# Performance work log

Hardware: AMD Instinct MI355X
Metric: run time of the kernel (lower is better)

Reference implementation:

```python
import jax, jax.numpy as jnp
import numpy as np

TOP_K = 2


def setup_inputs() -> dict:
    key = jax.random.key(0)
    k_x, k_g, k_w1, k_w2, k_w3 = jax.random.split(key, 5)
    B, S, D, H, E = 2, 512, 1024, 512, 8
    x = jax.random.normal(k_x, (B, S, D), dtype=jnp.float32)
    gate_w = jax.random.normal(k_g, (D, E), dtype=jnp.float32) * (D ** -0.5)
    w1 = jax.random.normal(k_w1, (E, D, H), dtype=jnp.float32) * 0.02  # gate proj
    w2 = jax.random.normal(k_w2, (E, H, D), dtype=jnp.float32) * 0.02  # down proj
    w3 = jax.random.normal(k_w3, (E, D, H), dtype=jnp.float32) * 0.02  # up proj
    return {"x": x, "gate_w": gate_w, "w1": w1, "w2": w2, "w3": w3}


def reference(x, gate_w, w1, w2, w3):
    # Token-choice top-k MoE with grouped SwiGLU experts, no shared expert.
    # Equivalent to torchtune MoE: gather routed tokens, scale by top-k router
    # score, run per-expert FFN, scatter-add back. Since each expert's FFN has
    # no bias (FFN(0) == 0), the dispatch/grouped-GEMM/combine is expressed
    # densely as sum_e FFN_e(scale[:, e] * x), which is mathematically identical.
    B, S, D = x.shape
    E = gate_w.shape[1]
    xf = x.reshape(B * S, D)                      # [T, D]
    T = B * S

    logits = xf @ gate_w                          # [T, E]
    scores = jax.nn.softmax(logits, axis=-1)
    top_scores, top_idx = jax.lax.top_k(scores, TOP_K)  # [T, k]

    # scale[t, e] = router score if expert e selected for token t, else 0
    scale = jnp.zeros((T, E), dtype=x.dtype).at[
        jnp.arange(T)[:, None], top_idx
    ].set(top_scores)

    xs = scale.T[:, :, None] * xf[None, :, :]     # [E, T, D] scaled routed input
    h = jax.nn.silu(jnp.einsum('etd,edh->eth', xs, w1)) \
        * jnp.einsum('etd,edh->eth', xs, w3)      # [E, T, H]
    y = jnp.einsum('eth,ehd->etd', h, w2)         # [E, T, D]
    out = y.sum(axis=0)                           # combine (scatter-add equiv)
    return out.reshape(B, S, D)
```

## Files before the change

### kernel.cpp

```cpp
#include <hip/hip_runtime.h>
#include <hip/hip_bf16.h>
#include <cstddef>

#define T_TOK 1024
#define D_DIM 1024
#define H_DIM 512
#define E_EXP 8
#define P_CAP 2560
#define MAX_MT (P_CAP / 64)
#define LDA 72

typedef __attribute__((ext_vector_type(4))) float    float4_t;
typedef __attribute__((ext_vector_type(4))) short    short4_t;
typedef __attribute__((ext_vector_type(8))) short    short8_t;
typedef __attribute__((ext_vector_type(4))) unsigned uint4_t;
typedef __attribute__((ext_vector_type(2))) unsigned uint2_t;

__device__ __forceinline__ short f2bf(float f) {
  union { float f; unsigned u; } v; v.f = f;
  unsigned u = v.u;
  u += 0x7FFFu + ((u >> 16) & 1u);
  return (short)(u >> 16);
}

__device__ __forceinline__ unsigned pkbf(float a, float b) {
  union { __hip_bfloat162 h; unsigned u; } v;
  v.h = __float22bfloat162_rn(make_float2(a, b));
  return v.u;
}

__global__ __launch_bounds__(256) void router_kernel(
    const float* __restrict__ x, const float* __restrict__ gw,
    int* __restrict__ idx2, float* __restrict__ scale2) {
  const int wid  = threadIdx.x >> 6;
  const int lane = threadIdx.x & 63;
  const int t = blockIdx.x * 4 + wid;
  const float* xr = x + (size_t)t * D_DIM;
  float acc[E_EXP];
  #pragma unroll
  for (int e = 0; e < E_EXP; ++e) acc[e] = 0.f;
  for (int d = lane; d < D_DIM; d += 64) {
    float xv = xr[d];
    float4_t g0 = *(const float4_t*)(gw + d * E_EXP);
    float4_t g1 = *(const float4_t*)(gw + d * E_EXP + 4);
    acc[0] += xv * g0[0]; acc[1] += xv * g0[1];
    acc[2] += xv * g0[2]; acc[3] += xv * g0[3];
    acc[4] += xv * g1[0]; acc[5] += xv * g1[1];
    acc[6] += xv * g1[2]; acc[7] += xv * g1[3];
  }
  #pragma unroll
  for (int off = 32; off >= 1; off >>= 1) {
    #pragma unroll
    for (int e = 0; e < E_EXP; ++e) acc[e] += __shfl_down(acc[e], off, 64);
  }
  if (lane == 0) {
    float m = acc[0];
    #pragma unroll
    for (int e = 1; e < E_EXP; ++e) m = fmaxf(m, acc[e]);
    float p[E_EXP]; float s = 0.f;
    #pragma unroll
    for (int e = 0; e < E_EXP; ++e) { p[e] = __expf(acc[e] - m); s += p[e]; }
    float inv = 1.f / s;
    #pragma unroll
    for (int e = 0; e < E_EXP; ++e) p[e] *= inv;
    int i1 = 0;
    #pragma unroll
    for (int e = 1; e < E_EXP; ++e) if (p[e] > p[i1]) i1 = e;
    int i2 = (i1 == 0) ? 1 : 0;
    #pragma unroll
    for (int e = 0; e < E_EXP; ++e) {
      if (e == i1 || e == i2) continue;
      if (p[e] > p[i2]) i2 = e;
    }
    idx2[2 * t]     = i1;  scale2[2 * t]     = p[i1];
    idx2[2 * t + 1] = i2;  scale2[2 * t + 1] = p[i2];
  }
}

__global__ __launch_bounds__(256) void scan_kernel(
    const int* __restrict__ idx2, const float* __restrict__ scale2,
    int* __restrict__ pair_tok, float* __restrict__ pair_scale,
    int* __restrict__ pairpos, int* __restrict__ meta) {
  __shared__ int cnt[E_EXP], base[E_EXP], cur[E_EXP];
  const int tid = threadIdx.x;
  if (tid < E_EXP) { cnt[tid] = 0; cur[tid] = 0; }
  for (int p = tid; p < P_CAP; p += 256) { pair_tok[p] = 0; pair_scale[p] = 0.f; }
  __syncthreads();
  for (int t = tid; t < T_TOK; t += 256) {
    atomicAdd(&cnt[idx2[2 * t]], 1);
    atomicAdd(&cnt[idx2[2 * t + 1]], 1);
  }
  __syncthreads();
  if (tid == 0) {
    int b = 0, g = 0;
    for (int e = 0; e < E_EXP; ++e) {
      base[e] = b;
      int al = (cnt[e] + 63) & ~63;
      for (int j = 0; j < al; j += 64) { meta[1 + g] = e; meta[41 + g] = b + j; ++g; }
      b += al;
    }
    meta[0] = g;
  }
  __syncthreads();
  for (int t = tid; t < T_TOK; t += 256) {
    #pragma unroll
    for (int s = 0; s < 2; ++s) {
      int e = idx2[2 * t + s];
      int p = base[e] + atomicAdd(&cur[e], 1);
      pair_tok[p] = t;
      pair_scale[p] = scale2[2 * t + s];
      pairpos[2 * t + s] = p;
    }
  }
}

__global__ __launch_bounds__(256, 2) void gemm1_kernel(
    const float* __restrict__ x, const float* __restrict__ w1,
    const float* __restrict__ w3,
    const int* __restrict__ pair_tok, const float* __restrict__ pair_scale,
    const int* __restrict__ meta, short* __restrict__ h) {
  __shared__ short As[64 * LDA], B1s[64 * LDA], B3s[64 * LDA];
  const int mt = blockIdx.y;
  if (mt >= meta[0]) return;
  const int e    = meta[1 + mt];
  const int row0 = meta[41 + mt];
  const int n0   = blockIdx.x * 64;
  const int tid = threadIdx.x, lane = tid & 63, wid = tid >> 6;
  const int wr = wid >> 1, wc = wid & 1;
  const int q = lane >> 4, ln = lane & 15;
  const float* w1e = w1 + (size_t)e * D_DIM * H_DIM;
  const float* w3e = w3 + (size_t)e * D_DIM * H_DIM;

  const int ar = tid >> 2, ak = tid & 3;
  const int   tok = pair_tok[row0 + ar];
  const float sc  = pair_scale[row0 + ar];
  const float* xrow = x + (size_t)tok * D_DIM + ak * 16;

  const int bk = tid >> 4, bn = tid & 15;

  float4_t acc1[2][2], acc3[2][2];
  #pragma unroll
  for (int i = 0; i < 2; ++i)
    #pragma unroll
    for (int j = 0; j < 2; ++j) {
      acc1[i][j] = (float4_t){0.f, 0.f, 0.f, 0.f};
      acc3[i][j] = (float4_t){0.f, 0.f, 0.f, 0.f};
    }

  for (int k0 = 0; k0 < D_DIM; k0 += 64) {
    {
      float4_t v0 = *(const float4_t*)(xrow + k0);
      float4_t v1 = *(const float4_t*)(xrow + k0 + 4);
      float4_t v2 = *(const float4_t*)(xrow + k0 + 8);
      float4_t v3 = *(const float4_t*)(xrow + k0 + 12);
      uint4_t u0 = {pkbf(v0[0] * sc, v0[1] * sc), pkbf(v0[2] * sc, v0[3] * sc),
                    pkbf(v1[0] * sc, v1[1] * sc), pkbf(v1[2] * sc, v1[3] * sc)};
      uint4_t u1 = {pkbf(v2[0] * sc, v2[1] * sc), pkbf(v2[2] * sc, v2[3] * sc),
                    pkbf(v3[0] * sc, v3[1] * sc), pkbf(v3[2] * sc, v3[3] * sc)};
      *(uint4_t*)&As[ar * LDA + ak * 16]     = u0;
      *(uint4_t*)&As[ar * LDA + ak * 16 + 8] = u1;
    }
    {
      const float* p1 = w1e + (size_t)(k0 + bk * 4) * H_DIM + n0 + bn * 4;
      const float* p3 = w3e + (size_t)(k0 + bk * 4) * H_DIM + n0 + bn * 4;
      float4_t a0 = *(const float4_t*)(p1);
      float4_t a1 = *(const float4_t*)(p1 + H_DIM);
      float4_t a2 = *(const float4_t*)(p1 + 2 * H_DIM);
      float4_t a3 = *(const float4_t*)(p1 + 3 * H_DIM);
      float4_t c0 = *(const float4_t*)(p3);
      float4_t c1 = *(const float4_t*)(p3 + H_DIM);
      float4_t c2 = *(const float4_t*)(p3 + 2 * H_DIM);
      float4_t c3 = *(const float4_t*)(p3 + 3 * H_DIM);
      #pragma unroll
      for (int i = 0; i < 4; ++i) {
        uint2_t u1v = {pkbf(a0[i], a1[i]), pkbf(a2[i], a3[i])};
        uint2_t u3v = {pkbf(c0[i], c1[i]), pkbf(c2[i], c3[i])};
        *(uint2_t*)&B1s[(bn * 4 + i) * LDA + bk * 4] = u1v;
        *(uint2_t*)&B3s[(bn * 4 + i) * LDA + bk * 4] = u3v;
      }
    }
    __syncthreads();

    short8_t af[2][2], b1f[2][2], b3f[2][2];
    #pragma unroll
    for (int i = 0; i < 2; ++i)
      #pragma unroll
      for (int kk = 0; kk < 2; ++kk)
        af[i][kk] = *(const short8_t*)&As[(wr * 32 + i * 16 + ln) * LDA + kk * 32 + q * 8];
    #pragma unroll
    for (int j = 0; j < 2; ++j)
      #pragma unroll
      for (int kk = 0; kk < 2; ++kk) {
        b1f[j][kk] = *(const short8_t*)&B1s[(wc * 32 + j * 16 + ln) * LDA + kk * 32 + q * 8];
        b3f[j][kk] = *(const short8_t*)&B3s[(wc * 32 + j * 16 + ln) * LDA + kk * 32 + q * 8];
      }
    #pragma unroll
    for (int i = 0; i < 2; ++i)
      #pragma unroll
      for (int j = 0; j < 2; ++j)
        #pragma unroll
        for (int kk = 0; kk < 2; ++kk) {
          acc1[i][j] = __builtin_amdgcn_mfma_f32_16x16x32_bf16(af[i][kk], b1f[j][kk], acc1[i][j], 0, 0, 0);
          acc3[i][j] = __builtin_amdgcn_mfma_f32_16x16x32_bf16(af[i][kk], b3f[j][kk], acc3[i][j], 0, 0, 0);
        }
    __syncthreads();
  }

  #pragma unroll
  for (int i = 0; i < 2; ++i) {
    int r_base = row0 + wr * 32 + i * 16 + q * 4;
    #pragma unroll
    for (int j = 0; j < 2; ++j) {
      int col = n0 + wc * 32 + j * 16 + ln;
      #pragma unroll
      for (int rr = 0; rr < 4; ++rr) {
        float c1 = acc1[i][j][rr];
        float c3 = acc3[i][j][rr];
        float sig = 1.f / (1.f + __expf(-c1));
        h[(size_t)(r_base + rr) * H_DIM + col] = f2bf(c1 * sig * c3);
      }
    }
  }
}

__global__ __launch_bounds__(256, 2) void gemm2_kernel(
    const short* __restrict__ h, const float* __restrict__ w2,
    const int* __restrict__ meta, float* __restrict__ y) {
  __shared__ short As[64 * LDA], Bs[64 * LDA];
  const int mt = blockIdx.y;
  if (mt >= meta[0]) return;
  const int e    = meta[1 + mt];
  const int row0 = meta[41 + mt];
  const int n0   = blockIdx.x * 64;
  const int tid = threadIdx.x, lane = tid & 63, wid = tid >> 6;
  const int wr = wid >> 1, wc = wid & 1;
  const int q = lane >> 4, ln = lane & 15;
  const float* w2e = w2 + (size_t)e * H_DIM * D_DIM;

  const int ar = tid >> 2, ak = tid & 3;
  const short* hrow = h + (size_t)(row0 + ar) * H_DIM + ak * 16;
  const int bk = tid >> 4, bn = tid & 15;

  float4_t acc[2][2];
  #pragma unroll
  for (int i = 0; i < 2; ++i)
    #pragma unroll
    for (int j = 0; j < 2; ++j) acc[i][j] = (float4_t){0.f, 0.f, 0.f, 0.f};

  for (int k0 = 0; k0 < H_DIM; k0 += 64) {
    {
      uint4_t u0 = *(const uint4_t*)(hrow + k0);
      uint4_t u1 = *(const uint4_t*)(hrow + k0 + 8);
      *(uint4_t*)&As[ar * LDA + ak * 16]     = u0;
      *(uint4_t*)&As[ar * LDA + ak * 16 + 8] = u1;
    }
    {
      const float* pb = w2e + (size_t)(k0 + bk * 4) * D_DIM + n0 + bn * 4;
      float4_t a0 = *(const float4_t*)(pb);
      float4_t a1 = *(const float4_t*)(pb + D_DIM);
      float4_t a2 = *(const float4_t*)(pb + 2 * D_DIM);
      float4_t a3 = *(const float4_t*)(pb + 3 * D_DIM);
      #pragma unroll
      for (int i = 0; i < 4; ++i) {
        uint2_t u = {pkbf(a0[i], a1[i]), pkbf(a2[i], a3[i])};
        *(uint2_t*)&Bs[(bn * 4 + i) * LDA + bk * 4] = u;
      }
    }
    __syncthreads();

    short8_t af[2][2], bf[2][2];
    #pragma unroll
    for (int i = 0; i < 2; ++i)
      #pragma unroll
      for (int kk = 0; kk < 2; ++kk)
        af[i][kk] = *(const short8_t*)&As[(wr * 32 + i * 16 + ln) * LDA + kk * 32 + q * 8];
    #pragma unroll
    for (int j = 0; j < 2; ++j)
      #pragma unroll
      for (int kk = 0; kk < 2; ++kk)
        bf[j][kk] = *(const short8_t*)&Bs[(wc * 32 + j * 16 + ln) * LDA + kk * 32 + q * 8];
    #pragma unroll
    for (int i = 0; i < 2; ++i)
      #pragma unroll
      for (int j = 0; j < 2; ++j)
        #pragma unroll
        for (int kk = 0; kk < 2; ++kk)
          acc[i][j] = __builtin_amdgcn_mfma_f32_16x16x32_bf16(af[i][kk], bf[j][kk], acc[i][j], 0, 0, 0);
    __syncthreads();
  }

  #pragma unroll
  for (int i = 0; i < 2; ++i) {
    int r_base = row0 + wr * 32 + i * 16 + q * 4;
    #pragma unroll
    for (int j = 0; j < 2; ++j) {
      int col = n0 + wc * 32 + j * 16 + ln;
      #pragma unroll
      for (int rr = 0; rr < 4; ++rr)
        y[(size_t)(r_base + rr) * D_DIM + col] = acc[i][j][rr];
    }
  }
}

__global__ __launch_bounds__(256) void combine_kernel(
    const float* __restrict__ y, const int* __restrict__ pairpos,
    float* __restrict__ out) {
  const int wid  = threadIdx.x >> 6;
  const int lane = threadIdx.x & 63;
  const int t = blockIdx.x * 4 + wid;
  const int p0 = pairpos[2 * t], p1 = pairpos[2 * t + 1];
  const float4_t* y0 = (const float4_t*)(y + (size_t)p0 * D_DIM);
  const float4_t* y1 = (const float4_t*)(y + (size_t)p1 * D_DIM);
  float4_t* o = (float4_t*)(out + (size_t)t * D_DIM);
  #pragma unroll
  for (int c = lane; c < D_DIM / 4; c += 64) o[c] = y0[c] + y1[c];
}

extern "C" void kernel_launch(void* const* d_in, const int* in_sizes, int n_in,
                              void* d_out, int out_size, void* d_ws, size_t ws_size,
                              hipStream_t stream) {
  const float* x  = (const float*)d_in[0];
  const float* gw = (const float*)d_in[1];
  const float* w1 = (const float*)d_in[2];
  const float* w2 = (const float*)d_in[3];
  const float* w3 = (const float*)d_in[4];
  float* out = (float*)d_out;

  char* ws = (char*)d_ws;
  int*   idx2    = (int*)  (ws);
  float* scale2  = (float*)(ws + 8192);
  int*   pairpos = (int*)  (ws + 16384);
  int*   ptok    = (int*)  (ws + 24576);
  float* pscale  = (float*)(ws + 40960);
  int*   meta    = (int*)  (ws + 57344);
  short* h       = (short*)(ws + 65536);
  float* y       = (float*)(ws + 65536 + (size_t)P_CAP * H_DIM * 2);

  router_kernel<<<dim3(T_TOK / 4), dim3(256), 0, stream>>>(x, gw, idx2, scale2);
  scan_kernel<<<dim3(1), dim3(256), 0, stream>>>(idx2, scale2, ptok, pscale, pairpos, meta);
  gemm1_kernel<<<dim3(H_DIM / 64, MAX_MT), dim3(256), 0, stream>>>(
      x, w1, w3, ptok, pscale, meta, h);
  gemm2_kernel<<<dim3(D_DIM / 64, MAX_MT), dim3(256), 0, stream>>>(h, w2, meta, y);
  combine_kernel<<<dim3(T_TOK / 4), dim3(256), 0, stream>>>(y, pairpos, out);
}
```

Baseline: 152.3 us.

## Pre-convert weights to transposed bf16 and fuse combine via atomic scatter-add

Adds a weight conversion kernel that transposes w1/w3/w2 to bf16 K-contiguous layout each call, so the GEMM kernels load B tiles with plain 16-byte copies instead of converting fp32 in the inner loop. Removes the intermediate y buffer and combine kernel: gemm2 now scatters results into a zeroed output with float atomicAdd, using pair_tok with -1 marking padding rows. The conversion re-reads and writes all expert weights each call (extra passes over about 50MB), and atomics make the summation order nondeterministic.

Measured after the change: 158.3 us. 1.04x slower.

```diff
diff --git a/kernel.cpp b/kernel.cpp
--- a/kernel.cpp
+++ b/kernel.cpp
@@ -27,6 +27,36 @@
   union { __hip_bfloat162 h; unsigned u; } v;
   v.h = __float22bfloat162_rn(make_float2(a, b));
   return v.u;
+}
+
+__global__ __launch_bounds__(256) void wconv_kernel(
+    const float* __restrict__ src, short* __restrict__ dst,
+    int K, int N, int ld_dst, int row_off, size_t src_es, size_t dst_es) {
+  __shared__ float tile[64][68];
+  const int e  = blockIdx.z;
+  const int k0 = blockIdx.x * 64;
+  const int n0 = blockIdx.y * 64;
+  const int tid = threadIdx.x;
+  const float* s = src + (size_t)e * src_es;
+  const int kr = tid >> 4, nc = (tid & 15) * 4;
+  #pragma unroll
+  for (int p = 0; p < 4; ++p) {
+    int k = p * 16 + kr;
+    float4_t v = *(const float4_t*)(s + (size_t)(k0 + k) * N + n0 + nc);
+    *(float4_t*)&tile[k][nc] = v;
+  }
+  __syncthreads();
+  const int r8 = tid >> 3, c8 = tid & 7;
+  short* d = dst + (size_t)e * dst_es;
+  #pragma unroll
+  for (int p = 0; p < 2; ++p) {
+    int row = p * 32 + r8;
+    uint4_t u;
+    #pragma unroll
+    for (int j = 0; j < 4; ++j)
+      u[j] = pkbf(tile[c8 * 8 + 2 * j][row], tile[c8 * 8 + 2 * j + 1][row]);
+    *(uint4_t*)(d + (size_t)(row_off + n0 + row) * ld_dst + k0 + c8 * 8) = u;
+  }
 }
 
 __global__ __launch_bounds__(256) void router_kernel(
@@ -80,11 +110,11 @@
 __global__ __launch_bounds__(256) void scan_kernel(
     const int* __restrict__ idx2, const float* __restrict__ scale2,
     int* __restrict__ pair_tok, float* __restrict__ pair_scale,
-    int* __restrict__ pairpos, int* __restrict__ meta) {
+    int* __restrict__ meta) {
   __shared__ int cnt[E_EXP], base[E_EXP], cur[E_EXP];
   const int tid = threadIdx.x;
   if (tid < E_EXP) { cnt[tid] = 0; cur[tid] = 0; }
-  for (int p = tid; p < P_CAP; p += 256) { pair_tok[p] = 0; pair_scale[p] = 0.f; }
+  for (int p = tid; p < P_CAP; p += 256) { pair_tok[p] = -1; pair_scale[p] = 0.f; }
   __syncthreads();
   for (int t = tid; t < T_TOK; t += 256) {
     atomicAdd(&cnt[idx2[2 * t]], 1);
@@ -109,14 +139,12 @@
       int p = base[e] + atomicAdd(&cur[e], 1);
       pair_tok[p] = t;
       pair_scale[p] = scale2[2 * t + s];
-      pairpos[2 * t + s] = p;
     }
   }
 }
 
 __global__ __launch_bounds__(256, 2) void gemm1_kernel(
-    const float* __restrict__ x, const float* __restrict__ w1,
-    const float* __restrict__ w3,
+    const float* __restrict__ x, const short* __restrict__ w13t,
     const int* __restrict__ pair_tok, const float* __restrict__ pair_scale,
     const int* __restrict__ meta, short* __restrict__ h) {
   __shared__ short As[64 * LDA], B1s[64 * LDA], B3s[64 * LDA];
@@ -128,15 +156,14 @@
   const int tid = threadIdx.x, lane = tid & 63, wid = tid >> 6;
   const int wr = wid >> 1, wc = wid & 1;
   const int q = lane >> 4, ln = lane & 15;
-  const float* w1e = w1 + (size_t)e * D_DIM * H_DIM;
-  const float* w3e = w3 + (size_t)e * D_DIM * H_DIM;
+  const short* bsrc = w13t + (size_t)e * D_DIM * (2 * H_DIM);
 
   const int ar = tid >> 2, ak = tid & 3;
-  const int   tok = pair_tok[row0 + ar];
-  const float sc  = pair_scale[row0 + ar];
-  const float* xrow = x + (size_t)tok * D_DIM + ak * 16;
-
-  const int bk = tid >> 4, bn = tid & 15;
+  const int   tokr = pair_tok[row0 + ar];
+  const float sc   = pair_scale[row0 + ar];
+  const float* xrow = x + (size_t)(tokr < 0 ? 0 : tokr) * D_DIM + ak * 16;
+
+  const int br = tid >> 3, bu = tid & 7;
 
   float4_t acc1[2][2], acc3[2][2];
   #pragma unroll
@@ -160,24 +187,13 @@
       *(uint4_t*)&As[ar * LDA + ak * 16]     = u0;
       *(uint4_t*)&As[ar * LDA + ak * 16 + 8] = u1;
     }
-    {
-      const float* p1 = w1e + (size_t)(k0 + bk * 4) * H_DIM + n0 + bn * 4;
-      const float* p3 = w3e + (size_t)(k0 + bk * 4) * H_DIM + n0 + bn * 4;
-      float4_t a0 = *(const float4_t*)(p1);
-      float4_t a1 = *(const float4_t*)(p1 + H_DIM);
-      float4_t a2 = *(const float4_t*)(p1 + 2 * H_DIM);
-      float4_t a3 = *(const float4_t*)(p1 + 3 * H_DIM);
-      float4_t c0 = *(const float4_t*)(p3);
-      float4_t c1 = *(const float4_t*)(p3 + H_DIM);
-      float4_t c2 = *(const float4_t*)(p3 + 2 * H_DIM);
-      float4_t c3 = *(const float4_t*)(p3 + 3 * H_DIM);
-      #pragma unroll
-      for (int i = 0; i < 4; ++i) {
-        uint2_t u1v = {pkbf(a0[i], a1[i]), pkbf(a2[i], a3[i])};
-        uint2_t u3v = {pkbf(c0[i], c1[i]), pkbf(c2[i], c3[i])};
-        *(uint2_t*)&B1s[(bn * 4 + i) * LDA + bk * 4] = u1v;
-        *(uint2_t*)&B3s[(bn * 4 + i) * LDA + bk * 4] = u3v;
-      }
+    #pragma unroll
+    for (int p = 0; p < 2; ++p) {
+      int row = p * 32 + br;
+      uint4_t v1 = *(const uint4_t*)(bsrc + (size_t)(n0 + row) * D_DIM + k0 + bu * 8);
+      uint4_t v3 = *(const uint4_t*)(bsrc + (size_t)(H_DIM + n0 + row) * D_DIM + k0 + bu * 8);
+      *(uint4_t*)&B1s[row * LDA + bu * 8] = v1;
+      *(uint4_t*)&B3s[row * LDA + bu * 8] = v3;
     }
     __syncthreads();
 
@@ -224,8 +240,9 @@
 }
 
 __global__ __launch_bounds__(256, 2) void gemm2_kernel(
-    const short* __restrict__ h, const float* __restrict__ w2,
-    const int* __restrict__ meta, float* __restrict__ y) {
+    const short* __restrict__ h, const short* __restrict__ w2t,
+    const int* __restrict__ pair_tok, const int* __restrict__ meta,
+    float* __restrict__ out) {
   __shared__ short As[64 * LDA], Bs[64 * LDA];
   const int mt = blockIdx.y;
   if (mt >= meta[0]) return;
@@ -235,11 +252,11 @@
   const int tid = threadIdx.x, lane = tid & 63, wid = tid >> 6;
   const int wr = wid >> 1, wc = wid & 1;
   const int q = lane >> 4, ln = lane & 15;
-  const float* w2e = w2 + (size_t)e * H_DIM * D_DIM;
+  const short* bsrc = w2t + (size_t)e * D_DIM * H_DIM;
 
   const int ar = tid >> 2, ak = tid & 3;
   const short* hrow = h + (size_t)(row0 + ar) * H_DIM + ak * 16;
-  const int bk = tid >> 4, bn = tid & 15;
+  const int br = tid >> 3, bu = tid & 7;
 
   float4_t acc[2][2];
   #pragma unroll
@@ -254,17 +271,11 @@
       *(uint4_t*)&As[ar * LDA + ak * 16]     = u0;
       *(uint4_t*)&As[ar * LDA + ak * 16 + 8] = u1;
     }
-    {
-      const float* pb = w2e + (size_t)(k0 + bk * 4) * D_DIM + n0 + bn * 4;
-      float4_t a0 = *(const float4_t*)(pb);
-      float4_t a1 = *(const float4_t*)(pb + D_DIM);
-      float4_t a2 = *(const float4_t*)(pb + 2 * D_DIM);
-      float4_t a3 = *(const float4_t*)(pb + 3 * D_DIM);
-      #pragma unroll
-      for (int i = 0; i < 4; ++i) {
-        uint2_t u = {pkbf(a0[i], a1[i]), pkbf(a2[i], a3[i])};
-        *(uint2_t*)&Bs[(bn * 4 + i) * LDA + bk * 4] = u;
-      }
+    #pragma unroll
+    for (int p = 0; p < 2; ++p) {
+      int row = p * 32 + br;
+      uint4_t v = *(const uint4_t*)(bsrc + (size_t)(n0 + row) * H_DIM + k0 + bu * 8);
+      *(uint4_t*)&Bs[row * LDA + bu * 8] = v;
     }
     __syncthreads();
 
@@ -293,27 +304,17 @@
   for (int i = 0; i < 2; ++i) {
     int r_base = row0 + wr * 32 + i * 16 + q * 4;
     #pragma unroll
-    for (int j = 0; j < 2; ++j) {
-      int col = n0 + wc * 32 + j * 16 + ln;
-      #pragma unroll
-      for (int rr = 0; rr < 4; ++rr)
-        y[(size_t)(r_base + rr) * D_DIM + col] = acc[i][j][rr];
-    }
-  }
-}
-
-__global__ __launch_bounds__(256) void combine_kernel(
-    const float* __restrict__ y, const int* __restrict__ pairpos,
-    float* __restrict__ out) {
-  const int wid  = threadIdx.x >> 6;
-  const int lane = threadIdx.x & 63;
-  const int t = blockIdx.x * 4 + wid;
-  const int p0 = pairpos[2 * t], p1 = pairpos[2 * t + 1];
-  const float4_t* y0 = (const float4_t*)(y + (size_t)p0 * D_DIM);
-  const float4_t* y1 = (const float4_t*)(y + (size_t)p1 * D_DIM);
-  float4_t* o = (float4_t*)(out + (size_t)t * D_DIM);
-  #pragma unroll
-  for (int c = lane; c < D_DIM / 4; c += 64) o[c] = y0[c] + y1[c];
+    for (int rr = 0; rr < 4; ++rr) {
+      int tok = pair_tok[r_base + rr];
+      if (tok < 0) continue;
+      float* orow = out + (size_t)tok * D_DIM;
+      #pragma unroll
+      for (int j = 0; j < 2; ++j) {
+        int col = n0 + wc * 32 + j * 16 + ln;
+        atomicAdd(orow + col, acc[i][j][rr]);
+      }
+    }
+  }
 }
 
 extern "C" void kernel_launch(void* const* d_in, const int* in_sizes, int n_in,
@@ -329,17 +330,27 @@
   char* ws = (char*)d_ws;
   int*   idx2    = (int*)  (ws);
   float* scale2  = (float*)(ws + 8192);
-  int*   pairpos = (int*)  (ws + 16384);
-  int*   ptok    = (int*)  (ws + 24576);
-  float* pscale  = (float*)(ws + 40960);
-  int*   meta    = (int*)  (ws + 57344);
+  int*   ptok    = (int*)  (ws + 16384);
+  float* pscale  = (float*)(ws + 32768);
+  int*   meta    = (int*)  (ws + 49152);
   short* h       = (short*)(ws + 65536);
-  float* y       = (float*)(ws + 65536 + (size_t)P_CAP * H_DIM * 2);
+  short* w13t    = (short*)(ws + 65536 + (size_t)P_CAP * H_DIM * 2);
+  short* w2t     = w13t + (size_t)E_EXP * D_DIM * 2 * H_DIM;
+
+  wconv_kernel<<<dim3(16, 8, E_EXP), dim3(256), 0, stream>>>(
+      w1, w13t, D_DIM, H_DIM, D_DIM, 0,     (size_t)D_DIM * H_DIM, (size_t)D_DIM * 2 * H_DIM);
+  wconv_kernel<<<dim3(16, 8, E_EXP), dim3(256), 0, stream>>>(
+      w3, w13t, D_DIM, H_DIM, D_DIM, H_DIM, (size_t)D_DIM * H_DIM, (size_t)D_DIM * 2 * H_DIM);
+  wconv_kernel<<<dim3(8, 16, E_EXP), dim3(256), 0, stream>>>(
+      w2, w2t, H_DIM, D_DIM, H_DIM, 0,      (size_t)H_DIM * D_DIM, (size_t)D_DIM * H_DIM);
 
   router_kernel<<<dim3(T_TOK / 4), dim3(256), 0, stream>>>(x, gw, idx2, scale2);
-  scan_kernel<<<dim3(1), dim3(256), 0, stream>>>(idx2, scale2, ptok, pscale, pairpos, meta);
+  scan_kernel<<<dim3(1), dim3(256), 0, stream>>>(idx2, scale2, ptok, pscale, meta);
+
   gemm1_kernel<<<dim3(H_DIM / 64, MAX_MT), dim3(256), 0, stream>>>(
-      x, w1, w3, ptok, pscale, meta, h);
-  gemm2_kernel<<<dim3(D_DIM / 64, MAX_MT), dim3(256), 0, stream>>>(h, w2, meta, y);
-  combine_kernel<<<dim3(T_TOK / 4), dim3(256), 0, stream>>>(y, pairpos, out);
-}
+      x, w13t, ptok, pscale, meta, h);
+
+  hipMemsetAsync(out, 0, (size_t)T_TOK * D_DIM * sizeof(float), stream);
+  gemm2_kernel<<<dim3(D_DIM / 64, MAX_MT), dim3(256), 0, stream>>>(
+      h, w2t, ptok, meta, out);
+}
```
